# Performance work log

Measured on AMD Instinct MI355X. Metric: run time of the kernel, lower is better.

Reference implementation:

```python
import jax, jax.numpy as jnp
import numpy as np

NSITES = 100000
NYEARS = 20
NVIS = 2
HDIM = 64


def setup_inputs() -> dict:
    key = jax.random.key(0)
    ks = jax.random.split(key, 10)
    def w(k, shape, fan_in):
        return (jax.random.normal(k, shape, jnp.float32) / np.sqrt(fan_in)).astype(jnp.float32)
    return {
        "sxy0": jax.random.normal(ks[0], (1, NSITES, 1), jnp.float32),
        "sxy": jax.random.normal(ks[1], (NSITES, NYEARS - 1, 1), jnp.float32),
        "oxy": jax.random.normal(ks[2], (NSITES, NYEARS, NVIS), jnp.float32),
        # to_h0: Linear(1 -> 64)
        "W_h0": w(ks[3], (HDIM, 1), 1), "b_h0": jnp.zeros((HDIM,), jnp.float32),
        # to_h1: Linear(64 -> 64)
        "W_h1": w(ks[4], (HDIM, HDIM), HDIM), "b_h1": jnp.zeros((HDIM,), jnp.float32),
        # to_hrnn: RNN(input=1, hidden=64, relu)
        "W_ih": w(ks[5], (HDIM, 1), 1), "b_ih": jnp.zeros((HDIM,), jnp.float32),
        "W_hh": w(ks[6], (HDIM, HDIM), HDIM), "b_hh": jnp.zeros((HDIM,), jnp.float32),
        # to_psi0 / to_psi: Linear(64 -> 1)
        "W_psi0": w(ks[7], (1, HDIM), HDIM), "b_psi0": jnp.zeros((1,), jnp.float32),
        "W_psi": w(ks[8], (1, HDIM), HDIM), "b_psi": jnp.zeros((1,), jnp.float32),
        # to_p: Linear(65 -> 1)
        "W_p": w(ks[9], (1, HDIM + 1), HDIM + 1), "b_p": jnp.zeros((1,), jnp.float32),
    }


def reference(sxy0, sxy, oxy, W_h0, b_h0, W_h1, b_h1, W_ih, b_ih, W_hh, b_hh,
              W_psi0, b_psi0, W_psi, b_psi, W_p, b_p):
    # site embeddings -> initial hidden state
    hs = jax.nn.elu(sxy0 @ W_h0.T + b_h0)            # [1, N, H]
    h0 = jax.nn.elu(hs @ W_h1.T + b_h1)              # [1, N, H]

    # single-layer relu RNN, batch_first: sxy [N, T, 1], h0 [1, N, H]
    xs = jnp.swapaxes(sxy, 0, 1)                     # [T, N, 1]
    def step(h, x):
        h_new = jax.nn.relu(x @ W_ih.T + b_ih + h @ W_hh.T + b_hh)
        return h_new, h_new
    _, h_seq = jax.lax.scan(step, h0[0], xs)         # [T, N, H]
    h_out = jnp.swapaxes(h_seq, 0, 1)                # [N, T, H]

    psi0_out = jax.nn.sigmoid(h0 @ W_psi0.T + b_psi0)   # [1, N, 1]
    psi_out = jax.nn.sigmoid(h_out @ W_psi.T + b_psi)   # [N, T, 1]

    # detection prob p[i, t, j] = sigmoid(to_p(cat(H[i, t], oxy[i, t, j])))
    # where H[:, 0] = h0 and H[:, t] = h_out[:, t-1] for t >= 1
    H = jnp.concatenate([h0[0][:, None, :], h_out], axis=1)  # [N, Y, H]
    logits = H @ W_p[:, :HDIM].T + oxy * W_p[0, HDIM] + b_p  # [N, Y, NVIS]
    p = jax.nn.sigmoid(logits)
    return psi0_out, psi_out, p
```

## Files before the change

### kernel.cpp

```cpp
#include <hip/hip_runtime.h>
#include <math.h>

#define NSITES 100000
#define NYEARS 20
#define HDIM 64

typedef __bf16 bf16x8 __attribute__((ext_vector_type(8)));
typedef float f32x4 __attribute__((ext_vector_type(4)));

__device__ __forceinline__ float sigmoidf_(float x) { return 1.0f / (1.0f + __expf(-x)); }
__device__ __forceinline__ float eluf_(float x) { return x > 0.0f ? x : expm1f(x); }

__device__ __forceinline__ bf16x8 cvt8_(const float* p) {
    float4 a = ((const float4*)p)[0];
    float4 b = ((const float4*)p)[1];
    bf16x8 r;
    r[0] = (__bf16)a.x; r[1] = (__bf16)a.y; r[2] = (__bf16)a.z; r[3] = (__bf16)a.w;
    r[4] = (__bf16)b.x; r[5] = (__bf16)b.y; r[6] = (__bf16)b.z; r[7] = (__bf16)b.w;
    return r;
}

__device__ __forceinline__ bf16x8 pack_bf_(f32x4 lo, f32x4 hi) {
    bf16x8 r;
    r[0] = (__bf16)lo[0]; r[1] = (__bf16)lo[1]; r[2] = (__bf16)lo[2]; r[3] = (__bf16)lo[3];
    r[4] = (__bf16)hi[0]; r[5] = (__bf16)hi[1]; r[6] = (__bf16)hi[2]; r[7] = (__bf16)hi[3];
    return r;
}

__global__ __launch_bounds__(64, 2)
void rnet_kernel(const float* __restrict__ sxy0,
                 const float* __restrict__ sxy,
                 const float* __restrict__ oxy,
                 const float* __restrict__ W_h0, const float* __restrict__ b_h0,
                 const float* __restrict__ W_h1, const float* __restrict__ b_h1,
                 const float* __restrict__ W_ih, const float* __restrict__ b_ih,
                 const float* __restrict__ W_hh, const float* __restrict__ b_hh,
                 const float* __restrict__ W_psi0, const float* __restrict__ b_psi0,
                 const float* __restrict__ W_psi, const float* __restrict__ b_psi,
                 const float* __restrict__ W_p, const float* __restrict__ b_p,
                 float* __restrict__ out)
{
    const int lane = threadIdx.x;
    const int s = lane & 15;
    const int q = lane >> 4;
    const int sq = s >> 2, sr = s & 3;
    const int base = blockIdx.x * 32;
    const int site0 = base + s;
    const int site1 = base + 16 + s;

    __shared__ __align__(16) float pL_sh[32 * 20];
    __shared__ __align__(16) float psiL_sh[32 * 19];

    float* __restrict__ out_psi0 = out;
    float* __restrict__ out_psi  = out + NSITES;
    float* __restrict__ out_p    = out + 20 * NSITES;

    bf16x8 a_hh[4][2];
#pragma unroll
    for (int mt = 0; mt < 4; ++mt) {
        const int ar = 32 * (mt >> 1) + 8 * sq + 4 * (mt & 1) + sr;
#pragma unroll
        for (int kt = 0; kt < 2; ++kt)
            a_hh[mt][kt] = cvt8_(W_hh + ar * 64 + kt * 32 + q * 8);
    }
    bf16x8 a_head[2];
    {
        const float* hrow = (s == 1) ? W_p : ((s == 2) ? W_psi0 : W_psi);
#pragma unroll
        for (int kt = 0; kt < 2; ++kt) a_head[kt] = cvt8_(hrow + kt * 32 + q * 8);
    }

    f32x4 biasD[4], wihD[4];
#pragma unroll
    for (int mt = 0; mt < 4; ++mt) {
        const int dr = 32 * (mt >> 1) + 8 * q + 4 * (mt & 1);
        float4 bi = *(const float4*)(b_ih + dr);
        float4 bh = *(const float4*)(b_hh + dr);
        float4 wi = *(const float4*)(W_ih + dr);
        biasD[mt][0] = bi.x + bh.x; biasD[mt][1] = bi.y + bh.y;
        biasD[mt][2] = bi.z + bh.z; biasD[mt][3] = bi.w + bh.w;
        wihD[mt][0] = wi.x; wihD[mt][1] = wi.y; wihD[mt][2] = wi.z; wihD[mt][3] = wi.w;
    }
    f32x4 headC;
    headC[0] = (q == 0) ? b_psi[0]  : 0.0f;
    headC[1] = (q == 0) ? b_p[0]    : 0.0f;
    headC[2] = (q == 0) ? b_psi0[0] : 0.0f;
    headC[3] = 0.0f;
    const float wpo = W_p[HDIM];

    float xs[2][NYEARS - 1];
#pragma unroll
    for (int i = 0; i < NYEARS - 1; ++i) {
        xs[0][i] = sxy[(size_t)site0 * (NYEARS - 1) + i];
        xs[1][i] = sxy[(size_t)site1 * (NYEARS - 1) + i];
    }

    bf16x8 bf[2][2];
    {
        float s0v[2];
        s0v[0] = sxy0[site0];
        s0v[1] = sxy0[site1];
        bf16x8 bf0[2][2];
#pragma unroll
        for (int kt = 0; kt < 2; ++kt) {
            const float* wp = W_h0 + kt * 32 + q * 8;
            const float* bp = b_h0 + kt * 32 + q * 8;
            float4 w0 = ((const float4*)wp)[0], w1 = ((const float4*)wp)[1];
            float4 c0 = ((const float4*)bp)[0], c1 = ((const float4*)bp)[1];
#pragma unroll
            for (int g = 0; g < 2; ++g) {
                const float sv = s0v[g];
                float v[8];
                v[0] = eluf_(fmaf(sv, w0.x, c0.x)); v[1] = eluf_(fmaf(sv, w0.y, c0.y));
                v[2] = eluf_(fmaf(sv, w0.z, c0.z)); v[3] = eluf_(fmaf(sv, w0.w, c0.w));
                v[4] = eluf_(fmaf(sv, w1.x, c1.x)); v[5] = eluf_(fmaf(sv, w1.y, c1.y));
                v[6] = eluf_(fmaf(sv, w1.z, c1.z)); v[7] = eluf_(fmaf(sv, w1.w, c1.w));
#pragma unroll
                for (int j = 0; j < 8; ++j) bf0[g][kt][j] = (__bf16)v[j];
            }
        }

        f32x4 acc[2][4];
#pragma unroll
        for (int mt = 0; mt < 4; ++mt) {
            const int dr = 32 * (mt >> 1) + 8 * q + 4 * (mt & 1);
            float4 b1 = *(const float4*)(b_h1 + dr);
#pragma unroll
            for (int g = 0; g < 2; ++g) {
                acc[g][mt][0] = b1.x; acc[g][mt][1] = b1.y;
                acc[g][mt][2] = b1.z; acc[g][mt][3] = b1.w;
            }
        }
#pragma unroll
        for (int kt = 0; kt < 2; ++kt)
#pragma unroll
            for (int mt = 0; mt < 4; ++mt) {
                const int ar = 32 * (mt >> 1) + 8 * sq + 4 * (mt & 1) + sr;
                bf16x8 a = cvt8_(W_h1 + ar * 64 + kt * 32 + q * 8);
#pragma unroll
                for (int g = 0; g < 2; ++g)
                    acc[g][mt] = __builtin_amdgcn_mfma_f32_16x16x32_bf16(a, bf0[g][kt], acc[g][mt], 0, 0, 0);
            }
#pragma unroll
        for (int g = 0; g < 2; ++g) {
            f32x4 e[4];
#pragma unroll
            for (int mt = 0; mt < 4; ++mt)
#pragma unroll
                for (int r = 0; r < 4; ++r) e[mt][r] = eluf_(acc[g][mt][r]);
            bf[g][0] = pack_bf_(e[0], e[1]);
            bf[g][1] = pack_bf_(e[2], e[3]);
        }
    }

#pragma unroll
    for (int t = 1; t < NYEARS; ++t) {
        f32x4 acc[2][4], accH[2];
#pragma unroll
        for (int g = 0; g < 2; ++g) {
            accH[g] = headC;
#pragma unroll
            for (int mt = 0; mt < 4; ++mt) acc[g][mt] = biasD[mt];
        }
#pragma unroll
        for (int kt = 0; kt < 2; ++kt) {
#pragma unroll
            for (int mt = 0; mt < 4; ++mt)
#pragma unroll
                for (int g = 0; g < 2; ++g)
                    acc[g][mt] = __builtin_amdgcn_mfma_f32_16x16x32_bf16(a_hh[mt][kt], bf[g][kt], acc[g][mt], 0, 0, 0);
#pragma unroll
            for (int g = 0; g < 2; ++g)
                accH[g] = __builtin_amdgcn_mfma_f32_16x16x32_bf16(a_head[kt], bf[g][kt], accH[g], 0, 0, 0);
        }

#pragma unroll
        for (int g = 0; g < 2; ++g) {
            const float x = xs[g][t - 1];
            f32x4 hn[4];
#pragma unroll
            for (int mt = 0; mt < 4; ++mt)
#pragma unroll
                for (int r = 0; r < 4; ++r)
                    hn[mt][r] = fmaxf(fmaf(x, wihD[mt][r], acc[g][mt][r]), 0.0f);
            bf[g][0] = pack_bf_(hn[0], hn[1]);
            bf[g][1] = pack_bf_(hn[2], hn[3]);

            if (q == 0) {
                const int ls = g * 16 + s;
                pL_sh[ls * 20 + (t - 1)] = accH[g][1];
                if (t == 1) {
                    out_psi0[base + g * 16 + s] = sigmoidf_(accH[g][2]);
                } else {
                    psiL_sh[ls * 19 + (t - 2)] = accH[g][0];
                }
            }
        }
    }

#pragma unroll
    for (int g = 0; g < 2; ++g) {
        f32x4 accH = headC;
#pragma unroll
        for (int kt = 0; kt < 2; ++kt)
            accH = __builtin_amdgcn_mfma_f32_16x16x32_bf16(a_head[kt], bf[g][kt], accH, 0, 0, 0);
        if (q == 0) {
            const int ls = g * 16 + s;
            pL_sh[ls * 20 + 19] = accH[1];
            psiL_sh[ls * 19 + 18] = accH[0];
        }
    }

    __syncthreads();

#pragma unroll
    for (int r = 0; r < 10; ++r) {
        int i = r * 64 + lane;
        if (i < 32 * 19)
            out_psi[(size_t)base * 19 + i] = sigmoidf_(psiL_sh[i]);
    }
    const float4* oxy_b = (const float4*)(oxy + (size_t)base * 40);
    float4* outp_b = (float4*)(out_p + (size_t)base * 40);
#pragma unroll
    for (int r = 0; r < 5; ++r) {
        int i4 = r * 64 + lane;
        float4 ox = oxy_b[i4];
        float lg0 = pL_sh[i4 * 2];
        float lg1 = pL_sh[i4 * 2 + 1];
        float4 pv;
        pv.x = sigmoidf_(fmaf(wpo, ox.x, lg0));
        pv.y = sigmoidf_(fmaf(wpo, ox.y, lg0));
        pv.z = sigmoidf_(fmaf(wpo, ox.z, lg1));
        pv.w = sigmoidf_(fmaf(wpo, ox.w, lg1));
        outp_b[i4] = pv;
    }
}

extern "C" void kernel_launch(void* const* d_in, const int* in_sizes, int n_in,
                              void* d_out, int out_size, void* d_ws, size_t ws_size,
                              hipStream_t stream) {
    const float* sxy0   = (const float*)d_in[0];
    const float* sxy    = (const float*)d_in[1];
    const float* oxy    = (const float*)d_in[2];
    const float* W_h0   = (const float*)d_in[3];
    const float* b_h0   = (const float*)d_in[4];
    const float* W_h1   = (const float*)d_in[5];
    const float* b_h1   = (const float*)d_in[6];
    const float* W_ih   = (const float*)d_in[7];
    const float* b_ih   = (const float*)d_in[8];
    const float* W_hh   = (const float*)d_in[9];
    const float* b_hh   = (const float*)d_in[10];
    const float* W_psi0 = (const float*)d_in[11];
    const float* b_psi0 = (const float*)d_in[12];
    const float* W_psi  = (const float*)d_in[13];
    const float* b_psi  = (const float*)d_in[14];
    const float* W_p    = (const float*)d_in[15];
    const float* b_p    = (const float*)d_in[16];

    float* out = (float*)d_out;

    dim3 block(64);
    dim3 grid(NSITES / 32);
    rnet_kernel<<<grid, block, 0, stream>>>(
        sxy0, sxy, oxy, W_h0, b_h0, W_h1, b_h1, W_ih, b_ih, W_hh, b_hh,
        W_psi0, b_psi0, W_psi, b_psi, W_p, b_p, out);
}
```

Before: 149.4 us.

## Stage sxy in LDS, stop unrolling time loop, reorder init and MFMA chain

Loads each block's sxy inputs into shared memory with coalesced lane-strided reads, replacing the per-thread register arrays of strided global loads. The recurrence loop is no longer unrolled, and each step's MFMA chain now starts from the bias registers instead of copying them into the accumulators first. The h0 computation is moved ahead of loading the recurrent weights to shorten register live ranges, and psi0 and psi logits are staged in shared memory for uniform indexing. The aim is lower register pressure, higher occupancy and better load coalescing, at the cost of loop overhead, an integer division in the output loop, and less scheduling freedom across time steps.

```diff
diff --git a/kernel.cpp b/kernel.cpp
--- a/kernel.cpp
+++ b/kernel.cpp
@@ -48,13 +48,82 @@
     const int site0 = base + s;
     const int site1 = base + 16 + s;
 
+    __shared__ __align__(16) float xs_sh[32 * 19];
     __shared__ __align__(16) float pL_sh[32 * 20];
-    __shared__ __align__(16) float psiL_sh[32 * 19];
+    __shared__ __align__(16) float psiL_sh[32 * 20];
+    __shared__ __align__(16) float psi0L_sh[32];
 
     float* __restrict__ out_psi0 = out;
     float* __restrict__ out_psi  = out + NSITES;
     float* __restrict__ out_p    = out + 20 * NSITES;
 
+    {
+        const float* src = sxy + (size_t)base * (NYEARS - 1);
+#pragma unroll
+        for (int r = 0; r < 10; ++r) {
+            int i = r * 64 + lane;
+            if (i < 32 * (NYEARS - 1)) xs_sh[i] = src[i];
+        }
+    }
+
+    bf16x8 bf[2][2];
+    {
+        float s0v[2];
+        s0v[0] = sxy0[site0];
+        s0v[1] = sxy0[site1];
+        bf16x8 bf0[2][2];
+#pragma unroll
+        for (int kt = 0; kt < 2; ++kt) {
+            const float* wp = W_h0 + kt * 32 + q * 8;
+            const float* bp = b_h0 + kt * 32 + q * 8;
+            float4 w0 = ((const float4*)wp)[0], w1 = ((const float4*)wp)[1];
+            float4 c0 = ((const float4*)bp)[0], c1 = ((const float4*)bp)[1];
+#pragma unroll
+            for (int g = 0; g < 2; ++g) {
+                const float sv = s0v[g];
+                float v[8];
+                v[0] = eluf_(fmaf(sv, w0.x, c0.x)); v[1] = eluf_(fmaf(sv, w0.y, c0.y));
+                v[2] = eluf_(fmaf(sv, w0.z, c0.z)); v[3] = eluf_(fmaf(sv, w0.w, c0.w));
+                v[4] = eluf_(fmaf(sv, w1.x, c1.x)); v[5] = eluf_(fmaf(sv, w1.y, c1.y));
+                v[6] = eluf_(fmaf(sv, w1.z, c1.z)); v[7] = eluf_(fmaf(sv, w1.w, c1.w));
+#pragma unroll
+                for (int j = 0; j < 8; ++j) bf0[g][kt][j] = (__bf16)v[j];
+            }
+        }
+
+        f32x4 acc[2][4];
+#pragma unroll
+        for (int mt = 0; mt < 4; ++mt) {
+            const int dr = 32 * (mt >> 1) + 8 * q + 4 * (mt & 1);
+            float4 b1 = *(const float4*)(b_h1 + dr);
+#pragma unroll
+            for (int g = 0; g < 2; ++g) {
+                acc[g][mt][0] = b1.x; acc[g][mt][1] = b1.y;
+                acc[g][mt][2] = b1.z; acc[g][mt][3] = b1.w;
+            }
+        }
+#pragma unroll
+        for (int kt = 0; kt < 2; ++kt)
+#pragma unroll
+            for (int mt = 0; mt < 4; ++mt) {
+                const int ar = 32 * (mt >> 1) + 8 * sq + 4 * (mt & 1) + sr;
+                bf16x8 a = cvt8_(W_h1 + ar * 64 + kt * 32 + q * 8);
+#pragma unroll
+                for (int g = 0; g < 2; ++g)
+                    acc[g][mt] = __builtin_amdgcn_mfma_f32_16x16x32_bf16(a, bf0[g][kt], acc[g][mt], 0, 0, 0);
+            }
+#pragma unroll
+        for (int g = 0; g < 2; ++g) {
+            f32x4 e[4];
+#pragma unroll
+            for (int mt = 0; mt < 4; ++mt)
+#pragma unroll
+                for (int r = 0; r < 4; ++r) e[mt][r] = eluf_(acc[g][mt][r]);
+            bf[g][0] = pack_bf_(e[0], e[1]);
+            bf[g][1] = pack_bf_(e[2], e[3]);
+        }
+    }
+
     bf16x8 a_hh[4][2];
 #pragma unroll
     for (int mt = 0; mt < 4; ++mt) {
@@ -69,7 +138,6 @@
 #pragma unroll
         for (int kt = 0; kt < 2; ++kt) a_head[kt] = cvt8_(hrow + kt * 32 + q * 8);
     }
-
     f32x4 biasD[4], wihD[4];
 #pragma unroll
     for (int mt = 0; mt < 4; ++mt) {
@@ -86,97 +154,31 @@
     headC[1] = (q == 0) ? b_p[0]    : 0.0f;
     headC[2] = (q == 0) ? b_psi0[0] : 0.0f;
     headC[3] = 0.0f;
-    const float wpo = W_p[HDIM];
-
-    float xs[2][NYEARS - 1];
-#pragma unroll
-    for (int i = 0; i < NYEARS - 1; ++i) {
-        xs[0][i] = sxy[(size_t)site0 * (NYEARS - 1) + i];
-        xs[1][i] = sxy[(size_t)site1 * (NYEARS - 1) + i];
-    }
-
-    bf16x8 bf[2][2];
-    {
-        float s0v[2];
-        s0v[0] = sxy0[site0];
-        s0v[1] = sxy0[site1];
-        bf16x8 bf0[2][2];
-#pragma unroll
-        for (int kt = 0; kt < 2; ++kt) {
-            const float* wp = W_h0 + kt * 32 + q * 8;
-            const float* bp = b_h0 + kt * 32 + q * 8;
-            float4 w0 = ((const float4*)wp)[0], w1 = ((const float4*)wp)[1];
-            float4 c0 = ((const float4*)bp)[0], c1 = ((const float4*)bp)[1];
-#pragma unroll
-            for (int g = 0; g < 2; ++g) {
-                const float sv = s0v[g];
-                float v[8];
-                v[0] = eluf_(fmaf(sv, w0.x, c0.x)); v[1] = eluf_(fmaf(sv, w0.y, c0.y));
-                v[2] = eluf_(fmaf(sv, w0.z, c0.z)); v[3] = eluf_(fmaf(sv, w0.w, c0.w));
-                v[4] = eluf_(fmaf(sv, w1.x, c1.x)); v[5] = eluf_(fmaf(sv, w1.y, c1.y));
-                v[6] = eluf_(fmaf(sv, w1.z, c1.z)); v[7] = eluf_(fmaf(sv, w1.w, c1.w));
-#pragma unroll
-                for (int j = 0; j < 8; ++j) bf0[g][kt][j] = (__bf16)v[j];
-            }
-        }
-
-        f32x4 acc[2][4];
+
+#pragma unroll 1
+    for (int t = 1; t < NYEARS; ++t) {
+        const float x0 = xs_sh[s * 19 + (t - 1)];
+        const float x1 = xs_sh[(16 + s) * 19 + (t - 1)];
+
+        f32x4 acc[2][4], accH[2];
 #pragma unroll
         for (int mt = 0; mt < 4; ++mt) {
-            const int dr = 32 * (mt >> 1) + 8 * q + 4 * (mt & 1);
-            float4 b1 = *(const float4*)(b_h1 + dr);
-#pragma unroll
-            for (int g = 0; g < 2; ++g) {
-                acc[g][mt][0] = b1.x; acc[g][mt][1] = b1.y;
-                acc[g][mt][2] = b1.z; acc[g][mt][3] = b1.w;
-            }
-        }
-#pragma unroll
-        for (int kt = 0; kt < 2; ++kt)
-#pragma unroll
-            for (int mt = 0; mt < 4; ++mt) {
-                const int ar = 32 * (mt >> 1) + 8 * sq + 4 * (mt & 1) + sr;
-                bf16x8 a = cvt8_(W_h1 + ar * 64 + kt * 32 + q * 8);
-#pragma unroll
-                for (int g = 0; g < 2; ++g)
-                    acc[g][mt] = __builtin_amdgcn_mfma_f32_16x16x32_bf16(a, bf0[g][kt], acc[g][mt], 0, 0, 0);
-            }
+            acc[0][mt] = __builtin_amdgcn_mfma_f32_16x16x32_bf16(a_hh[mt][0], bf[0][0], biasD[mt], 0, 0, 0);
+            acc[1][mt] = __builtin_amdgcn_mfma_f32_16x16x32_bf16(a_hh[mt][0], bf[1][0], biasD[mt], 0, 0, 0);
+        }
+        accH[0] = __builtin_amdgcn_mfma_f32_16x16x32_bf16(a_head[0], bf[0][0], headC, 0, 0, 0);
+        accH[1] = __builtin_amdgcn_mfma_f32_16x16x32_bf16(a_head[0], bf[1][0], headC, 0, 0, 0);
+#pragma unroll
+        for (int mt = 0; mt < 4; ++mt) {
+            acc[0][mt] = __builtin_amdgcn_mfma_f32_16x16x32_bf16(a_hh[mt][1], bf[0][1], acc[0][mt], 0, 0, 0);
+            acc[1][mt] = __builtin_amdgcn_mfma_f32_16x16x32_bf16(a_hh[mt][1], bf[1][1], acc[1][mt], 0, 0, 0);
+        }
+        accH[0] = __builtin_amdgcn_mfma_f32_16x16x32_bf16(a_head[1], bf[0][1], accH[0], 0, 0, 0);
+        accH[1] = __builtin_amdgcn_mfma_f32_16x16x32_bf16(a_head[1], bf[1][1], accH[1], 0, 0, 0);
+
 #pragma unroll
         for (int g = 0; g < 2; ++g) {
-            f32x4 e[4];
-#pragma unroll
-            for (int mt = 0; mt < 4; ++mt)
-#pragma unroll
-                for (int r = 0; r < 4; ++r) e[mt][r] = eluf_(acc[g][mt][r]);
-            bf[g][0] = pack_bf_(e[0], e[1]);
-            bf[g][1] = pack_bf_(e[2], e[3]);
-        }
-    }
-
-#pragma unroll
-    for (int t = 1; t < NYEARS; ++t) {
-        f32x4 acc[2][4], accH[2];
-#pragma unroll
-        for (int g = 0; g < 2; ++g) {
-            accH[g] = headC;
-#pragma unroll
-            for (int mt = 0; mt < 4; ++mt) acc[g][mt] = biasD[mt];
-        }
-#pragma unroll
-        for (int kt = 0; kt < 2; ++kt) {
-#pragma unroll
-            for (int mt = 0; mt < 4; ++mt)
-#pragma unroll
-                for (int g = 0; g < 2; ++g)
-                    acc[g][mt] = __builtin_amdgcn_mfma_f32_16x16x32_bf16(a_hh[mt][kt], bf[g][kt], acc[g][mt], 0, 0, 0);
-#pragma unroll
-            for (int g = 0; g < 2; ++g)
-                accH[g] = __builtin_amdgcn_mfma_f32_16x16x32_bf16(a_head[kt], bf[g][kt], accH[g], 0, 0, 0);
-        }
-
-#pragma unroll
-        for (int g = 0; g < 2; ++g) {
-            const float x = xs[g][t - 1];
+            const float x = g ? x1 : x0;
             f32x4 hn[4];
 #pragma unroll
             for (int mt = 0; mt < 4; ++mt)
@@ -185,39 +187,41 @@
                     hn[mt][r] = fmaxf(fmaf(x, wihD[mt][r], acc[g][mt][r]), 0.0f);
             bf[g][0] = pack_bf_(hn[0], hn[1]);
             bf[g][1] = pack_bf_(hn[2], hn[3]);
-
-            if (q == 0) {
+        }
+
+        if (q == 0) {
+#pragma unroll
+            for (int g = 0; g < 2; ++g) {
                 const int ls = g * 16 + s;
-                pL_sh[ls * 20 + (t - 1)] = accH[g][1];
-                if (t == 1) {
-                    out_psi0[base + g * 16 + s] = sigmoidf_(accH[g][2]);
-                } else {
-                    psiL_sh[ls * 19 + (t - 2)] = accH[g][0];
-                }
+                pL_sh[ls * 20 + (t - 1)]   = accH[g][1];
+                psiL_sh[ls * 20 + (t - 1)] = accH[g][0];
+                if (t == 1) psi0L_sh[ls] = accH[g][2];
             }
         }
     }
 
 #pragma unroll
     for (int g = 0; g < 2; ++g) {
-        f32x4 accH = headC;
-#pragma unroll
-        for (int kt = 0; kt < 2; ++kt)
-            accH = __builtin_amdgcn_mfma_f32_16x16x32_bf16(a_head[kt], bf[g][kt], accH, 0, 0, 0);
+        f32x4 accH = __builtin_amdgcn_mfma_f32_16x16x32_bf16(a_head[0], bf[g][0], headC, 0, 0, 0);
+        accH = __builtin_amdgcn_mfma_f32_16x16x32_bf16(a_head[1], bf[g][1], accH, 0, 0, 0);
         if (q == 0) {
             const int ls = g * 16 + s;
-            pL_sh[ls * 20 + 19] = accH[1];
-            psiL_sh[ls * 19 + 18] = accH[0];
+            pL_sh[ls * 20 + 19]   = accH[1];
+            psiL_sh[ls * 20 + 19] = accH[0];
         }
     }
 
     __syncthreads();
 
+    const float wpo = W_p[HDIM];
+    if (lane < 32) out_psi0[base + lane] = sigmoidf_(psi0L_sh[lane]);
 #pragma unroll
     for (int r = 0; r < 10; ++r) {
         int i = r * 64 + lane;
-        if (i < 32 * 19)
-            out_psi[(size_t)base * 19 + i] = sigmoidf_(psiL_sh[i]);
+        if (i < 32 * 19) {
+            int sl = i / 19, c = i - sl * 19;
+            out_psi[(size_t)base * 19 + i] = sigmoidf_(psiL_sh[sl * 20 + c + 1]);
+        }
     }
     const float4* oxy_b = (const float4*)(oxy + (size_t)base * 40);
     float4* outp_b = (float4*)(out_p + (size_t)base * 40);
```

After: 153.6 us. +2.8%, slower.
